# Performance work log

Hardware: AMD Instinct MI355X
Metric: run time of the kernel (lower is better)

## Reference

```python
import jax, jax.numpy as jnp
import numpy as np

D = 256        # emb_dim
H = 16         # num_heads
HD = D // H    # head_dim
N = 16384      # num users
B, S = 64, 128 # seq batch / length; M = B*S


def setup_inputs() -> dict:
    key = jax.random.key(0)
    ks = jax.random.split(key, 8)
    scale = 1.0 / np.sqrt(D)
    return {
        "user_feat": jax.random.normal(ks[0], (N, D), dtype=jnp.float32),
        "seq_feat": jax.random.normal(ks[1], (B, S, D), dtype=jnp.float32),
        "in_proj_w": jax.random.uniform(ks[2], (3 * D, D), jnp.float32, -scale, scale),
        "in_proj_b": jnp.zeros((3 * D,), jnp.float32),
        "out_proj_w": jax.random.uniform(ks[3], (D, D), jnp.float32, -scale, scale),
        "out_proj_b": jnp.zeros((D,), jnp.float32),
        "trans_w": jax.random.uniform(ks[4], (D, D), jnp.float32, -scale, scale),
        "trans_b": jax.random.uniform(ks[5], (D,), jnp.float32, -scale, scale),
    }


def _mha(x, in_proj_w, in_proj_b, out_proj_w, out_proj_b):
    # x: [B, S, D] self-attention, batch_first, like nn.MultiheadAttention
    qkv = jnp.einsum("bsd,ed->bse", x, in_proj_w) + in_proj_b  # [B,S,3D]
    q, k, v = jnp.split(qkv, 3, axis=-1)
    def heads(t):  # [B,S,D] -> [B,H,S,HD]
        return t.reshape(B, S, H, HD).transpose(0, 2, 1, 3)
    q, k, v = heads(q), heads(k), heads(v)
    scores = jnp.einsum("bhqd,bhkd->bhqk", q, k) / np.sqrt(HD)
    attn = jax.nn.softmax(scores, axis=-1)
    out = jnp.einsum("bhqk,bhkd->bhqd", attn, v)  # [B,H,S,HD]
    out = out.transpose(0, 2, 1, 3).reshape(B, S, D)
    return out @ out_proj_w.T + out_proj_b


def reference(user_feat, seq_feat, in_proj_w, in_proj_b, out_proj_w, out_proj_b, trans_w, trans_b):
    seq = _mha(seq_feat, in_proj_w, in_proj_b, out_proj_w, out_proj_b)
    seq = seq.reshape(-1, D)                        # [M, D]
    M = seq.shape[0]
    att = user_feat @ seq.T                         # [N, M]
    att = att / jnp.maximum(jnp.sum(jnp.abs(att), axis=1, keepdims=True), 1e-12)  # F.normalize p=1
    # mean_j Linear(att_ij * seq_j) == Linear((att @ seq) / M)  (exact, by linearity)
    agg = (att @ seq) / M                           # [N, D]
    return user_feat + (agg @ trans_w.T + trans_b)
```

## Files before the change

kernel.cpp:

```cpp
#include <hip/hip_runtime.h>


typedef __bf16 bf16_t;
typedef __bf16 bf16x8 __attribute__((ext_vector_type(8)));
typedef __bf16 bf16x4 __attribute__((ext_vector_type(4)));
typedef float  f32x4  __attribute__((ext_vector_type(4)));
typedef unsigned int u32x4 __attribute__((ext_vector_type(4)));

#define MFMA16(a, b, c) __builtin_amdgcn_mfma_f32_16x16x32_bf16((a), (b), (c), 0, 0, 0)

#define AS1 __attribute__((address_space(1)))
#define AS3 __attribute__((address_space(3)))
#define GLOAD_LDS16(g, l) \
    __builtin_amdgcn_global_load_lds((const AS1 unsigned int*)(const void*)(g), \
                                     (AS3 unsigned int*)(void*)(l), 16, 0, 0)

__device__ __forceinline__ int swz256(int row, int k) { return row * 256 + (k ^ ((row & 7) << 3)); }

__global__ void k_cvt(const float* __restrict__ s, bf16_t* __restrict__ d, int n4) {
    int i  = blockIdx.x * blockDim.x + threadIdx.x;
    int st = gridDim.x * blockDim.x;
    for (; i < n4; i += st) {
        float4 v = ((const float4*)s)[i];
        bf16x4 o = { (bf16_t)v.x, (bf16_t)v.y, (bf16_t)v.z, (bf16_t)v.w };
        ((bf16x4*)d)[i] = o;
    }
}

__global__ __launch_bounds__(256, 1)
void k_gemm_bt(const bf16_t* __restrict__ A, const bf16_t* __restrict__ B,
               const float* __restrict__ bias, bf16_t* __restrict__ Cb, int N) {
    __shared__ bf16_t Al[64 * 256];
    __shared__ bf16_t Bl[64 * 256];
    const int tid  = threadIdx.x;
    const int lane = tid & 63;
    const int w    = tid >> 6;
    const int l15  = lane & 15;
    const int l4   = lane >> 4;
    const int rb = blockIdx.y * 64, cb = blockIdx.x * 64;

    {
        const u32x4* sa = (const u32x4*)(A + (size_t)rb * 256);
        const u32x4* sb = (const u32x4*)(B + (size_t)cb * 256);
        u32x4* da = (u32x4*)Al;
        u32x4* db = (u32x4*)Bl;
#pragma unroll
        for (int i = 0; i < 8; ++i) {
            int ch  = i * 256 + tid;
            int row = ch >> 5, cp = ch & 31;
            int sch = (ch & ~31) | (cp ^ (row & 7));
            da[sch] = sa[ch];
            db[sch] = sb[ch];
        }
    }
    __syncthreads();

    f32x4 acc[4];
#pragma unroll
    for (int n = 0; n < 4; ++n) acc[n] = (f32x4){0.f, 0.f, 0.f, 0.f};
#pragma unroll
    for (int t = 0; t < 8; ++t) {
        int k = t * 32 + l4 * 8;
        bf16x8 af = *(const bf16x8*)(Al + swz256(16 * w + l15, k));
#pragma unroll
        for (int n = 0; n < 4; ++n) {
            bf16x8 bfr = *(const bf16x8*)(Bl + swz256(16 * n + l15, k));
            acc[n] = MFMA16(af, bfr, acc[n]);
        }
    }
#pragma unroll
    for (int n = 0; n < 4; ++n) {
        int col = cb + 16 * n + l15;
        float bv = bias ? bias[col] : 0.f;
#pragma unroll
        for (int r = 0; r < 4; ++r) {
            int row = rb + 16 * w + l4 * 4 + r;
            Cb[(size_t)row * N + col] = (bf16_t)(acc[n][r] + bv);
        }
    }
}

__global__ __launch_bounds__(256, 1)
void k_gemm_seqT(const bf16_t* __restrict__ A, const bf16_t* __restrict__ B,
                 const float* __restrict__ bias, bf16_t* __restrict__ Cb,
                 bf16_t* __restrict__ CTb) {
    __shared__ bf16_t Al[64 * 256];
    __shared__ bf16_t Bl[64 * 256];
    __shared__ float  Tt[64][65];
    const int tid  = threadIdx.x;
    const int lane = tid & 63;
    const int w    = tid >> 6;
    const int l15  = lane & 15;
    const int l4   = lane >> 4;
    const int rb = blockIdx.y * 64, cb = blockIdx.x * 64;

    {
        const u32x4* sa = (const u32x4*)(A + (size_t)rb * 256);
        const u32x4* sb = (const u32x4*)(B + (size_t)cb * 256);
        u32x4* da = (u32x4*)Al;
        u32x4* db = (u32x4*)Bl;
#pragma unroll
        for (int i = 0; i < 8; ++i) {
            int ch  = i * 256 + tid;
            int row = ch >> 5, cp = ch & 31;
            int sch = (ch & ~31) | (cp ^ (row & 7));
            da[sch] = sa[ch];
            db[sch] = sb[ch];
        }
    }
    __syncthreads();

    f32x4 acc[4];
#pragma unroll
    for (int n = 0; n < 4; ++n) acc[n] = (f32x4){0.f, 0.f, 0.f, 0.f};
#pragma unroll
    for (int t = 0; t < 8; ++t) {
        int k = t * 32 + l4 * 8;
        bf16x8 af = *(const bf16x8*)(Al + swz256(16 * w + l15, k));
#pragma unroll
        for (int n = 0; n < 4; ++n) {
            bf16x8 bfr = *(const bf16x8*)(Bl + swz256(16 * n + l15, k));
            acc[n] = MFMA16(af, bfr, acc[n]);
        }
    }
#pragma unroll
    for (int n = 0; n < 4; ++n) {
        int col = cb + 16 * n + l15;
        float bv = bias[col];
#pragma unroll
        for (int r = 0; r < 4; ++r) {
            int row = rb + 16 * w + l4 * 4 + r;
            float v = acc[n][r] + bv;
            Cb[(size_t)row * 256 + col] = (bf16_t)v;
            Tt[16 * n + l15][16 * w + l4 * 4 + r] = v;
        }
    }
    __syncthreads();
#pragma unroll
    for (int i = 0; i < 16; ++i) {
        int e = i * 256 + tid;
        int lc = e >> 6, lr = e & 63;
        CTb[(size_t)(cb + lc) * 8192 + rb + lr] = (bf16_t)Tt[lc][lr];
    }
}

__global__ __launch_bounds__(128, 1)
void k_mha(const bf16_t* __restrict__ qkv, bf16_t* __restrict__ attn) {
    __shared__ float Kl[128][17];
    __shared__ float Vl[128][17];
    const int bh = blockIdx.x;
    const int b = bh >> 4, h = bh & 15;
    const int t = threadIdx.x;
    const size_t rowbase = (size_t)b * 128;

    const bf16_t* base = qkv + (rowbase + t) * 768 + h * 16;
    bf16x8 qa = *(const bf16x8*)(base),       qb = *(const bf16x8*)(base + 8);
    bf16x8 ka = *(const bf16x8*)(base + 256), kb = *(const bf16x8*)(base + 264);
    bf16x8 va = *(const bf16x8*)(base + 512), vb = *(const bf16x8*)(base + 520);
    float q[16];
#pragma unroll
    for (int e = 0; e < 8; ++e) {
        q[e] = (float)qa[e]; q[8 + e] = (float)qb[e];
        Kl[t][e] = (float)ka[e]; Kl[t][8 + e] = (float)kb[e];
        Vl[t][e] = (float)va[e]; Vl[t][8 + e] = (float)vb[e];
    }
    __syncthreads();

    float m = -1e30f;
    for (int j = 0; j < 128; ++j) {
        float s = 0.f;
#pragma unroll
        for (int d = 0; d < 16; ++d) s += q[d] * Kl[j][d];
        m = fmaxf(m, s * 0.25f);
    }
    float sum = 0.f;
    float o[16];
#pragma unroll
    for (int d = 0; d < 16; ++d) o[d] = 0.f;
    for (int j = 0; j < 128; ++j) {
        float s = 0.f;
#pragma unroll
        for (int d = 0; d < 16; ++d) s += q[d] * Kl[j][d];
        float e = __expf(s * 0.25f - m);
        sum += e;
#pragma unroll
        for (int d = 0; d < 16; ++d) o[d] += e * Vl[j][d];
    }
    float inv = 1.f / sum;
    bf16_t* out = attn + (rowbase + t) * 256 + h * 16;
#pragma unroll
    for (int d = 0; d < 16; ++d) out[d] = (bf16_t)(o[d] * inv);
}

__global__ __launch_bounds__(512, 2)
void k_rowabs(const bf16_t* __restrict__ Ub, const bf16_t* __restrict__ Sq,
              float* __restrict__ rsp) {
    __shared__ bf16_t Kl[2][64 * 256];

    const int tid  = threadIdx.x;
    const int lane = tid & 63;
    const int wid  = tid >> 6;
    const int wr   = wid >> 2;
    const int wc   = wid & 3;
    const int l15  = lane & 15;
    const int l4   = lane >> 4;
    const int q0   = blockIdx.x * 128;
    const int jy   = blockIdx.y;
    const int jbase = jy * 4096;

    int koff[4];
#pragma unroll
    for (int i = 0; i < 4; ++i) {
        int c = wid * 256 + i * 64 + lane;
        int sc = (c & ~31) | ((c & 31) ^ ((c >> 5) & 7));
        koff[i] = sc * 16;
    }
    auto stage = [&](int b, int j0) {
        const char* gK = (const char*)Sq + (size_t)j0 * 512;
        char* lK = (char*)(&Kl[b][0]) + wid * 4096;
#pragma unroll
        for (int i = 0; i < 4; ++i) GLOAD_LDS16(gK + koff[i], lK + i * 1024);
    };

    bf16x8 uf[4][8];
#pragma unroll
    for (int rt = 0; rt < 4; ++rt) {
        const bf16_t* up = Ub + (size_t)(q0 + 64 * wr + 16 * rt + l15) * 256 + l4 * 8;
#pragma unroll
        for (int t = 0; t < 8; ++t) uf[rt][t] = *(const bf16x8*)(up + t * 32);
    }

    float rsacc[4][4];
#pragma unroll
    for (int rt = 0; rt < 4; ++rt)
#pragma unroll
        for (int r = 0; r < 4; ++r) rsacc[rt][r] = 0.f;

    stage(0, jbase);
    __syncthreads();

    for (int it = 0; it < 64; ++it) {
        const int cur = it & 1;
        if (it + 1 < 64) stage(cur ^ 1, jbase + (it + 1) * 64);
        const bf16_t* Klc = &Kl[cur][0];

        f32x4 sacc[4];
#pragma unroll
        for (int rt = 0; rt < 4; ++rt) sacc[rt] = (f32x4){0.f, 0.f, 0.f, 0.f};
#pragma unroll
        for (int t = 0; t < 8; ++t) {
            int k = t * 32 + l4 * 8;
            bf16x8 bfr = *(const bf16x8*)(Klc + swz256(16 * wc + l15, k));
#pragma unroll
            for (int rt = 0; rt < 4; ++rt)
                sacc[rt] = MFMA16(uf[rt][t], bfr, sacc[rt]);
        }
#pragma unroll
        for (int rt = 0; rt < 4; ++rt)
#pragma unroll
            for (int r = 0; r < 4; ++r) rsacc[rt][r] += fabsf(sacc[rt][r]);
        __syncthreads();
    }

    float* rdst = rsp + (size_t)(jy * 4 + wc) * 16384 + q0 + 64 * wr;
#pragma unroll
    for (int rt = 0; rt < 4; ++rt)
#pragma unroll
        for (int r = 0; r < 4; ++r) {
            float v = rsacc[rt][r];
            v += __shfl_xor(v, 1, 16);
            v += __shfl_xor(v, 2, 16);
            v += __shfl_xor(v, 4, 16);
            v += __shfl_xor(v, 8, 16);
            if (l15 == 0) rdst[16 * rt + 4 * l4 + r] = v;
        }
}

__global__ void k_rs(const float* __restrict__ rsp, float* __restrict__ rs) {
    int i = blockIdx.x * blockDim.x + threadIdx.x;
    float s = 0.f;
#pragma unroll
    for (int p = 0; p < 8; ++p) s += rsp[(size_t)p * 16384 + i];
    rs[i] = 1.f / (fmaxf(s, 1e-12f) * 8192.f);
}

__global__ __launch_bounds__(256, 1)
void k_gram(const bf16_t* __restrict__ ST, float* __restrict__ Gpart) {
    __shared__ bf16_t Al[64 * 256];
    __shared__ bf16_t Bl[64 * 256];
    const int tid = threadIdx.x, lane = tid & 63, w = tid >> 6;
    const int l15 = lane & 15, l4 = lane >> 4;
    const int rb = blockIdx.y * 64, cb = blockIdx.x * 64;
    const int jb = blockIdx.z * 1024;

    f32x4 acc[4];
#pragma unroll
    for (int n = 0; n < 4; ++n) acc[n] = (f32x4){0.f, 0.f, 0.f, 0.f};

    for (int kt4 = 0; kt4 < 4; ++kt4) {
        int j0 = jb + kt4 * 256;
        __syncthreads();
        u32x4* da = (u32x4*)Al;
        u32x4* db = (u32x4*)Bl;
#pragma unroll
        for (int i = 0; i < 8; ++i) {
            int ch  = i * 256 + tid;
            int row = ch >> 5, cp = ch & 31;
            int sch = (ch & ~31) | (cp ^ (row & 7));
            da[sch] = *(const u32x4*)(ST + (size_t)(rb + row) * 8192 + j0 + cp * 8);
            db[sch] = *(const u32x4*)(ST + (size_t)(cb + row) * 8192 + j0 + cp * 8);
        }
        __syncthreads();
#pragma unroll
        for (int t = 0; t < 8; ++t) {
            int k = t * 32 + l4 * 8;
            bf16x8 af = *(const bf16x8*)(Al + swz256(16 * w + l15, k));
#pragma unroll
            for (int n = 0; n < 4; ++n) {
                bf16x8 bfr = *(const bf16x8*)(Bl + swz256(16 * n + l15, k));
                acc[n] = MFMA16(af, bfr, acc[n]);
            }
        }
    }
    float* gp = Gpart + (size_t)blockIdx.z * 65536;
#pragma unroll
    for (int n = 0; n < 4; ++n)
#pragma unroll
        for (int r = 0; r < 4; ++r)
            gp[(size_t)(rb + 16 * w + l4 * 4 + r) * 256 + cb + 16 * n + l15] = acc[n][r];
}

__global__ __launch_bounds__(256, 1)
void k_gh(const float* __restrict__ Gpart, const float* __restrict__ W,
          bf16_t* __restrict__ HT) {
    __shared__ bf16_t Al[64 * 256];
    __shared__ bf16_t Bl[64 * 256];
    const int tid = threadIdx.x, lane = tid & 63, w = tid >> 6;
    const int l15 = lane & 15, l4 = lane >> 4;
    const int rb = blockIdx.y * 64, cb = blockIdx.x * 64;

#pragma unroll
    for (int i = 0; i < 16; ++i) {
        int idx = i * 1024 + tid * 4;
        int row = idx >> 8, col = idx & 255;
        f32x4 s = *(const f32x4*)(Gpart + (size_t)(rb + row) * 256 + col);
#pragma unroll
        for (int p = 1; p < 8; ++p)
            s += *(const f32x4*)(Gpart + (size_t)p * 65536 + (size_t)(rb + row) * 256 + col);
        f32x4 wv = *(const f32x4*)(W + (size_t)(cb + row) * 256 + col);
        int sc = col ^ ((row & 7) << 3);
        bf16x4 ga = { (bf16_t)s[0], (bf16_t)s[1], (bf16_t)s[2], (bf16_t)s[3] };
        bf16x4 wb = { (bf16_t)wv[0], (bf16_t)wv[1], (bf16_t)wv[2], (bf16_t)wv[3] };
        *(bf16x4*)(Al + row * 256 + sc) = ga;
        *(bf16x4*)(Bl + row * 256 + sc) = wb;
    }
    __syncthreads();

    f32x4 acc[4];
#pragma unroll
    for (int n = 0; n < 4; ++n) acc[n] = (f32x4){0.f, 0.f, 0.f, 0.f};
#pragma unroll
    for (int t = 0; t < 8; ++t) {
        int k = t * 32 + l4 * 8;
        bf16x8 af = *(const bf16x8*)(Al + swz256(16 * w + l15, k));
#pragma unroll
        for (int n = 0; n < 4; ++n) {
            bf16x8 bfr = *(const bf16x8*)(Bl + swz256(16 * n + l15, k));
            acc[n] = MFMA16(af, bfr, acc[n]);
        }
    }
#pragma unroll
    for (int n = 0; n < 4; ++n)
#pragma unroll
        for (int r = 0; r < 4; ++r)
            HT[(size_t)(cb + 16 * n + l15) * 256 + rb + 16 * w + l4 * 4 + r] =
                (bf16_t)acc[n][r];
}

__global__ __launch_bounds__(256, 1)
void k_final(const bf16_t* __restrict__ A, const bf16_t* __restrict__ B,
             const float* __restrict__ rs, const float* __restrict__ tb,
             const float* __restrict__ user, float* __restrict__ out) {
    __shared__ bf16_t Al[64 * 256];
    __shared__ bf16_t Bl[64 * 256];
    const int tid  = threadIdx.x;
    const int lane = tid & 63;
    const int w    = tid >> 6;
    const int l15  = lane & 15;
    const int l4   = lane >> 4;
    const int rb = blockIdx.y * 64, cb = blockIdx.x * 64;

    {
        const u32x4* sa = (const u32x4*)(A + (size_t)rb * 256);
        const u32x4* sb = (const u32x4*)(B + (size_t)cb * 256);
        u32x4* da = (u32x4*)Al;
        u32x4* db = (u32x4*)Bl;
#pragma unroll
        for (int i = 0; i < 8; ++i) {
            int ch  = i * 256 + tid;
            int row = ch >> 5, cp = ch & 31;
            int sch = (ch & ~31) | (cp ^ (row & 7));
            da[sch] = sa[ch];
            db[sch] = sb[ch];
        }
    }
    __syncthreads();

    f32x4 acc[4];
#pragma unroll
    for (int n = 0; n < 4; ++n) acc[n] = (f32x4){0.f, 0.f, 0.f, 0.f};
#pragma unroll
    for (int t = 0; t < 8; ++t) {
        int k = t * 32 + l4 * 8;
        bf16x8 af = *(const bf16x8*)(Al + swz256(16 * w + l15, k));
#pragma unroll
        for (int n = 0; n < 4; ++n) {
            bf16x8 bfr = *(const bf16x8*)(Bl + swz256(16 * n + l15, k));
            acc[n] = MFMA16(af, bfr, acc[n]);
        }
    }
    float c[4];
#pragma unroll
    for (int r = 0; r < 4; ++r) c[r] = rs[rb + 16 * w + l4 * 4 + r];
#pragma unroll
    for (int n = 0; n < 4; ++n) {
        int col = cb + 16 * n + l15;
        float bv = tb[col];
#pragma unroll
        for (int r = 0; r < 4; ++r) {
            int row = rb + 16 * w + l4 * 4 + r;
            size_t idx = (size_t)row * 256 + col;
            out[idx] = user[idx] + c[r] * acc[n][r] + bv;
        }
    }
}

extern "C" void kernel_launch(void* const* d_in, const int* in_sizes, int n_in,
                              void* d_out, int out_size, void* d_ws, size_t ws_size,
                              hipStream_t stream) {
    const float* user_feat  = (const float*)d_in[0];
    const float* seq_feat   = (const float*)d_in[1];
    const float* in_proj_w  = (const float*)d_in[2];
    const float* in_proj_b  = (const float*)d_in[3];
    const float* out_proj_w = (const float*)d_in[4];
    const float* out_proj_b = (const float*)d_in[5];
    const float* trans_w    = (const float*)d_in[6];
    const float* trans_b    = (const float*)d_in[7];
    float* out = (float*)d_out;

    char* w = (char*)d_ws;
    size_t off = 0;
    auto take = [&](size_t bytes) { void* p = w + off; off += (bytes + 255) & ~(size_t)255; return p; };
    bf16_t* Ub    = (bf16_t*)take((size_t)16384 * 256 * 2);
    bf16_t* Xb    = (bf16_t*)take((size_t)8192 * 256 * 2);
    bf16_t* W1b   = (bf16_t*)take((size_t)768 * 256 * 2);
    bf16_t* W2b   = (bf16_t*)take((size_t)256 * 256 * 2);
    bf16_t* attnb = (bf16_t*)take((size_t)8192 * 256 * 2);
    bf16_t* seqb  = (bf16_t*)take((size_t)8192 * 256 * 2);
    bf16_t* seqTb = (bf16_t*)take((size_t)256 * 8192 * 2);
    char*   regA  = (char*)take((size_t)8192 * 768 * 4);
    bf16_t* qkvb  = (bf16_t*)regA;
    float*  Gpart = (float*)regA;
    bf16_t* HTb   = (bf16_t*)(regA + (size_t)8 * 65536 * 4);
    float*  rsp   = (float*)Xb;
    float*  rs    = (float*)(Xb + (size_t)8 * 16384 * 2);

    k_cvt<<<2048, 256, 0, stream>>>(user_feat, Ub, 16384 * 256 / 4);
    k_cvt<<<2048, 256, 0, stream>>>(seq_feat, Xb, 8192 * 256 / 4);
    k_cvt<<<192, 256, 0, stream>>>(in_proj_w, W1b, 768 * 256 / 4);
    k_cvt<<<64, 256, 0, stream>>>(out_proj_w, W2b, 256 * 256 / 4);

    k_gemm_bt<<<dim3(12, 128), 256, 0, stream>>>(Xb, W1b, in_proj_b, qkvb, 768);

    k_mha<<<1024, 128, 0, stream>>>(qkvb, attnb);

    k_gemm_seqT<<<dim3(4, 128), 256, 0, stream>>>(attnb, W2b, out_proj_b, seqb, seqTb);

    k_rowabs<<<dim3(128, 2), 512, 0, stream>>>(Ub, seqb, rsp);
    k_rs<<<64, 256, 0, stream>>>(rsp, rs);

    k_gram<<<dim3(4, 4, 8), 256, 0, stream>>>(seqTb, Gpart);
    k_gh<<<dim3(4, 4), 256, 0, stream>>>(Gpart, trans_w, HTb);

    k_final<<<dim3(4, 256), 256, 0, stream>>>(Ub, HTb, rs, trans_b, user_feat, out);
}
```

Measured before the change: 183.7 us.

## Fuse conversions, split MHA keys across halves, widen rowabs grid, fold rs into final

Merges the four fp32-to-bf16 conversion launches into one kernel. Splits each attention block's 128 keys across two thread halves, caching the scores so they are not recomputed, and combines the partial max, sum and output through LDS. Doubles the rowabs grid along the key dimension so more blocks run at once. Removes the k_rs kernel and computes the row-scale reduction inside k_final. The aim is fewer launches, more parallelism and less redundant work, at the cost of more registers in k_mha and more partial sums to read.

After: 389.6 us. 112% more time.

```diff
diff --git a/kernel.cpp b/kernel.cpp
--- a/kernel.cpp
+++ b/kernel.cpp
@@ -17,13 +17,24 @@
 
 __device__ __forceinline__ int swz256(int row, int k) { return row * 256 + (k ^ ((row & 7) << 3)); }
 
-__global__ void k_cvt(const float* __restrict__ s, bf16_t* __restrict__ d, int n4) {
+__global__ void k_cvt_all(const float* __restrict__ u, const float* __restrict__ x,
+                          const float* __restrict__ w1, const float* __restrict__ w2,
+                          bf16_t* __restrict__ ub, bf16_t* __restrict__ xb,
+                          bf16_t* __restrict__ w1b, bf16_t* __restrict__ w2b) {
+    const int NU = 16384 * 256 / 4, NX = 8192 * 256 / 4;
+    const int NW1 = 768 * 256 / 4, NW2 = 256 * 256 / 4;
+    const int total = NU + NX + NW1 + NW2;
     int i  = blockIdx.x * blockDim.x + threadIdx.x;
     int st = gridDim.x * blockDim.x;
-    for (; i < n4; i += st) {
-        float4 v = ((const float4*)s)[i];
+    for (; i < total; i += st) {
+        const float* s; bf16_t* d; int k;
+        if (i < NU)                { s = u;  d = ub;  k = i; }
+        else if (i < NU + NX)      { s = x;  d = xb;  k = i - NU; }
+        else if (i < NU + NX + NW1){ s = w1; d = w1b; k = i - NU - NX; }
+        else                       { s = w2; d = w2b; k = i - NU - NX - NW1; }
+        float4 v = ((const float4*)s)[k];
         bf16x4 o = { (bf16_t)v.x, (bf16_t)v.y, (bf16_t)v.z, (bf16_t)v.w };
-        ((bf16x4*)d)[i] = o;
+        ((bf16x4*)d)[k] = o;
     }
 }
 
@@ -144,55 +155,80 @@
     }
 }
 
-__global__ __launch_bounds__(128, 1)
+__global__ __launch_bounds__(256, 3)
 void k_mha(const bf16_t* __restrict__ qkv, bf16_t* __restrict__ attn) {
     __shared__ float Kl[128][17];
     __shared__ float Vl[128][17];
+    __shared__ float mx2[2][128];
+    __shared__ float sm1[128];
+    __shared__ float ol[128][17];
     const int bh = blockIdx.x;
     const int b = bh >> 4, h = bh & 15;
-    const int t = threadIdx.x;
+    const int tid  = threadIdx.x;
+    const int t    = tid & 127;
+    const int half = tid >> 7;
     const size_t rowbase = (size_t)b * 128;
-
-    const bf16_t* base = qkv + (rowbase + t) * 768 + h * 16;
-    bf16x8 qa = *(const bf16x8*)(base),       qb = *(const bf16x8*)(base + 8);
-    bf16x8 ka = *(const bf16x8*)(base + 256), kb = *(const bf16x8*)(base + 264);
-    bf16x8 va = *(const bf16x8*)(base + 512), vb = *(const bf16x8*)(base + 520);
+    const bf16_t* rowp = qkv + (rowbase + t) * 768 + h * 16;
+
+    {
+        const bf16_t* src = rowp + 256 + half * 256;
+        bf16x8 a = *(const bf16x8*)(src);
+        bf16x8 c = *(const bf16x8*)(src + 8);
+        float* dst = half ? &Vl[t][0] : &Kl[t][0];
+#pragma unroll
+        for (int e = 0; e < 8; ++e) { dst[e] = (float)a[e]; dst[8 + e] = (float)c[e]; }
+    }
     float q[16];
-#pragma unroll
-    for (int e = 0; e < 8; ++e) {
-        q[e] = (float)qa[e]; q[8 + e] = (float)qb[e];
-        Kl[t][e] = (float)ka[e]; Kl[t][8 + e] = (float)kb[e];
-        Vl[t][e] = (float)va[e]; Vl[t][8 + e] = (float)vb[e];
-    }
-    __syncthreads();
-
-    float m = -1e30f;
-    for (int j = 0; j < 128; ++j) {
-        float s = 0.f;
-#pragma unroll
-        for (int d = 0; d < 16; ++d) s += q[d] * Kl[j][d];
-        m = fmaxf(m, s * 0.25f);
-    }
+    {
+        bf16x8 qa = *(const bf16x8*)(rowp);
+        bf16x8 qb = *(const bf16x8*)(rowp + 8);
+#pragma unroll
+        for (int e = 0; e < 8; ++e) { q[e] = (float)qa[e]; q[8 + e] = (float)qb[e]; }
+    }
+    __syncthreads();
+
+    const int j0 = half * 64;
+    float s[64];
+    float mx = -1e30f;
+#pragma unroll
+    for (int j = 0; j < 64; ++j) {
+        float v = 0.f;
+#pragma unroll
+        for (int d = 0; d < 16; ++d) v += q[d] * Kl[j0 + j][d];
+        v *= 0.25f;
+        s[j] = v;
+        mx = fmaxf(mx, v);
+    }
+    mx2[half][t] = mx;
+    __syncthreads();
+    const float m = fmaxf(mx2[0][t], mx2[1][t]);
+
     float sum = 0.f;
     float o[16];
 #pragma unroll
     for (int d = 0; d < 16; ++d) o[d] = 0.f;
-    for (int j = 0; j < 128; ++j) {
-        float s = 0.f;
-#pragma unroll
-        for (int d = 0; d < 16; ++d) s += q[d] * Kl[j][d];
-        float e = __expf(s * 0.25f - m);
+#pragma unroll
+    for (int j = 0; j < 64; ++j) {
+        float e = __expf(s[j] - m);
         sum += e;
 #pragma unroll
-        for (int d = 0; d < 16; ++d) o[d] += e * Vl[j][d];
-    }
-    float inv = 1.f / sum;
-    bf16_t* out = attn + (rowbase + t) * 256 + h * 16;
-#pragma unroll
-    for (int d = 0; d < 16; ++d) out[d] = (bf16_t)(o[d] * inv);
-}
-
-__global__ __launch_bounds__(512, 2)
+        for (int d = 0; d < 16; ++d) o[d] += e * Vl[j0 + j][d];
+    }
+    if (half) {
+        sm1[t] = sum;
+#pragma unroll
+        for (int d = 0; d < 16; ++d) ol[t][d] = o[d];
+    }
+    __syncthreads();
+    if (!half) {
+        float inv = 1.f / (sum + sm1[t]);
+        bf16_t* outp = attn + (rowbase + t) * 256 + h * 16;
+#pragma unroll
+        for (int d = 0; d < 16; ++d) outp[d] = (bf16_t)((o[d] + ol[t][d]) * inv);
+    }
+}
+
+__global__ __launch_bounds__(512, 4)
 void k_rowabs(const bf16_t* __restrict__ Ub, const bf16_t* __restrict__ Sq,
               float* __restrict__ rsp) {
     __shared__ bf16_t Kl[2][64 * 256];
@@ -206,7 +242,7 @@
     const int l4   = lane >> 4;
     const int q0   = blockIdx.x * 128;
     const int jy   = blockIdx.y;
-    const int jbase = jy * 4096;
+    const int jbase = jy * 2048;
 
     int koff[4];
 #pragma unroll
@@ -239,9 +275,9 @@
     stage(0, jbase);
     __syncthreads();
 
-    for (int it = 0; it < 64; ++it) {
+    for (int it = 0; it < 32; ++it) {
         const int cur = it & 1;
-        if (it + 1 < 64) stage(cur ^ 1, jbase + (it + 1) * 64);
+        if (it + 1 < 32) stage(cur ^ 1, jbase + (it + 1) * 64);
         const bf16_t* Klc = &Kl[cur][0];
 
         f32x4 sacc[4];
@@ -274,14 +310,6 @@
             v += __shfl_xor(v, 8, 16);
             if (l15 == 0) rdst[16 * rt + 4 * l4 + r] = v;
         }
-}
-
-__global__ void k_rs(const float* __restrict__ rsp, float* __restrict__ rs) {
-    int i = blockIdx.x * blockDim.x + threadIdx.x;
-    float s = 0.f;
-#pragma unroll
-    for (int p = 0; p < 8; ++p) s += rsp[(size_t)p * 16384 + i];
-    rs[i] = 1.f / (fmaxf(s, 1e-12f) * 8192.f);
 }
 
 __global__ __launch_bounds__(256, 1)
@@ -379,10 +407,11 @@
 
 __global__ __launch_bounds__(256, 1)
 void k_final(const bf16_t* __restrict__ A, const bf16_t* __restrict__ B,
-             const float* __restrict__ rs, const float* __restrict__ tb,
+             const float* __restrict__ rsp, const float* __restrict__ tb,
              const float* __restrict__ user, float* __restrict__ out) {
     __shared__ bf16_t Al[64 * 256];
     __shared__ bf16_t Bl[64 * 256];
+    __shared__ float  crs[64];
     const int tid  = threadIdx.x;
     const int lane = tid & 63;
     const int w    = tid >> 6;
@@ -404,6 +433,12 @@
             db[sch] = sb[ch];
         }
     }
+    if (tid < 64) {
+        float s = 0.f;
+#pragma unroll
+        for (int p = 0; p < 16; ++p) s += rsp[(size_t)p * 16384 + rb + tid];
+        crs[tid] = 1.f / (fmaxf(s, 1e-12f) * 8192.f);
+    }
     __syncthreads();
 
     f32x4 acc[4];
@@ -421,7 +456,7 @@
     }
     float c[4];
 #pragma unroll
-    for (int r = 0; r < 4; ++r) c[r] = rs[rb + 16 * w + l4 * 4 + r];
+    for (int r = 0; r < 4; ++r) c[r] = crs[16 * w + l4 * 4 + r];
 #pragma unroll
     for (int n = 0; n < 4; ++n) {
         int col = cb + 16 * n + l15;
@@ -463,24 +498,20 @@
     float*  Gpart = (float*)regA;
     bf16_t* HTb   = (bf16_t*)(regA + (size_t)8 * 65536 * 4);
     float*  rsp   = (float*)Xb;
-    float*  rs    = (float*)(Xb + (size_t)8 * 16384 * 2);
-
-    k_cvt<<<2048, 256, 0, stream>>>(user_feat, Ub, 16384 * 256 / 4);
-    k_cvt<<<2048, 256, 0, stream>>>(seq_feat, Xb, 8192 * 256 / 4);
-    k_cvt<<<192, 256, 0, stream>>>(in_proj_w, W1b, 768 * 256 / 4);
-    k_cvt<<<64, 256, 0, stream>>>(out_proj_w, W2b, 256 * 256 / 4);
+
+    k_cvt_all<<<2048, 256, 0, stream>>>(user_feat, seq_feat, in_proj_w, out_proj_w,
+                                        Ub, Xb, W1b, W2b);
 
     k_gemm_bt<<<dim3(12, 128), 256, 0, stream>>>(Xb, W1b, in_proj_b, qkvb, 768);
 
-    k_mha<<<1024, 128, 0, stream>>>(qkvb, attnb);
+    k_mha<<<1024, 256, 0, stream>>>(qkvb, attnb);
 
     k_gemm_seqT<<<dim3(4, 128), 256, 0, stream>>>(attnb, W2b, out_proj_b, seqb, seqTb);
 
-    k_rowabs<<<dim3(128, 2), 512, 0, stream>>>(Ub, seqb, rsp);
-    k_rs<<<64, 256, 0, stream>>>(rsp, rs);
+    k_rowabs<<<dim3(128, 4), 512, 0, stream>>>(Ub, seqb, rsp);
 
     k_gram<<<dim3(4, 4, 8), 256, 0, stream>>>(seqTb, Gpart);
     k_gh<<<dim3(4, 4), 256, 0, stream>>>(Gpart, trans_w, HTb);
 
-    k_final<<<dim3(4, 256), 256, 0, stream>>>(Ub, HTb, rs, trans_b, user_feat, out);
-}
+    k_final<<<dim3(4, 256), 256, 0, stream>>>(Ub, HTb, rsp, trans_b, user_feat, out);
+}
```
